# Kernel tuning notes

Hardware: AMD Instinct MI355X
Metric: run time of the kernel (lower is better)

Reference implementation:

```python
import math
import jax, jax.numpy as jnp
import numpy as np

B, T, E, H = 8, 2048, 512, 8
NQ_H, NL = 4, 2          # qubits per attention head, circuit layers
NQ_F, FFN = 8, 2048      # FFN qubits, ffn_dim

# ---- batched state-vector quantum simulation -------------------------------
# state shape: [N, 2, 2, ..., 2] (one axis of size 2 per qubit; wire q = axis q+1)

def apply_ry(state, q, theta):
    """RY(theta) on wire q. theta: scalar or [N] (per-batch angle)."""
    th = jnp.asarray(theta) * 0.5
    c, s = jnp.cos(th), jnp.sin(th)
    if th.ndim == 1:
        shp = (-1,) + (1,) * (state.ndim - 2)
        c, s = c.reshape(shp), s.reshape(shp)
    s0 = jax.lax.index_in_dim(state, 0, axis=q + 1, keepdims=False)
    s1 = jax.lax.index_in_dim(state, 1, axis=q + 1, keepdims=False)
    return jnp.stack([c * s0 - s * s1, s * s0 + c * s1], axis=q + 1)

def apply_cnot(state, ctrl, tgt):
    c0 = jax.lax.index_in_dim(state, 0, axis=ctrl + 1, keepdims=True)
    c1 = jax.lax.index_in_dim(state, 1, axis=ctrl + 1, keepdims=True)
    c1 = jnp.flip(c1, axis=tgt + 1)  # X on target when control = 1
    return jnp.concatenate([c0, c1], axis=ctrl + 1)

def run_circuit(x, params):
    """x: [N, n] data angles. params: [L, n] (shared) or [N, L, n] (per-element).
    Circuit: L x (RY(params) layer + CNOT chain + ring CNOT), then RY(x), then <Z_q>.
    Returns [N, n] PauliZ expectations."""
    N, n = x.shape
    L = params.shape[-2]
    state = jnp.zeros((N, 2 ** n), x.dtype).at[:, 0].set(1.0).reshape((N,) + (2,) * n)
    for l in range(L):
        for q in range(n):
            theta = params[:, l, q] if params.ndim == 3 else params[l, q]
            state = apply_ry(state, q, theta)
        for q in range(n - 1):
            state = apply_cnot(state, q, q + 1)
        state = apply_cnot(state, n - 1, 0)
    for q in range(n):
        state = apply_ry(state, q, x[:, q])
    probs = (state ** 2).reshape(N, 2 ** n)
    bits = (jnp.arange(2 ** n)[:, None] >> (n - 1 - jnp.arange(n))) & 1  # wire 0 = MSB
    return probs @ (1 - 2 * bits).astype(x.dtype)  # [N, n]

def layer_norm(x, g, b, eps=1e-5):
    m = x.mean(-1, keepdims=True)
    v = ((x - m) ** 2).mean(-1, keepdims=True)
    return (x - m) / jnp.sqrt(v + eps) * g + b

def setup_inputs() -> dict:
    key = jax.random.key(0)
    ks = jax.random.split(key, 9)
    def lin(k, o, i):
        return jax.random.normal(k, (o, i), jnp.float32) / np.sqrt(i).astype(np.float32)
    return {
        "x": jax.random.normal(ks[0], (B, T, E), jnp.float32),
        "wq": lin(ks[1], E, E), "wk": lin(ks[2], E, E),
        "wv": lin(ks[3], E, E), "wo": lin(ks[4], E, E),
        "head_params": jax.random.normal(ks[5], (H, NL, NQ_H), jnp.float32),
        "ffn_params": jax.random.normal(ks[6], (2, NQ_F), jnp.float32),
        "w1": lin(ks[7], FFN, NQ_F), "w2": lin(ks[8], E, FFN),
        "g1": jnp.ones((E,), jnp.float32), "b1": jnp.zeros((E,), jnp.float32),
        "g2": jnp.ones((E,), jnp.float32), "b2": jnp.zeros((E,), jnp.float32),
    }

def reference(x, wq, wk, wv, wo, head_params, ffn_params, w1, w2, g1, b1, g2, b2):
    Bb, Tt, Ee = x.shape
    hd = Ee // H
    BT = Bb * Tt
    # ---- quantum multi-head attention (dropout = eval/identity) ----
    q = x @ wq.T; k = x @ wk.T; v = x @ wv.T
    scores = jnp.einsum('bte,bse->bts', q, k) / math.sqrt(Ee)  # NOTE: scale by sqrt(E)
    attn = jax.nn.softmax(scores, axis=-1)
    out = jnp.einsum('bts,bse->bte', attn, v)                  # [B,T,E]
    oh = out.reshape(Bb, Tt, H, hd)
    # fold heads into the batch dim; per-head params broadcast per element
    xh = oh[..., :NQ_H].transpose(2, 0, 1, 3).reshape(H * BT, NQ_H)
    ph = jnp.broadcast_to(head_params[:, None], (H, BT, NL, NQ_H)).reshape(H * BT, NL, NQ_H)
    qout = run_circuit(xh, ph)                                  # [H*BT, NQ_H]
    qout = jnp.pad(qout, ((0, 0), (0, hd - NQ_H)))              # zero-pad to head_dim
    qout = qout.reshape(H, Bb, Tt, hd).transpose(1, 2, 0, 3).reshape(Bb, Tt, Ee)
    attn_out = qout @ wo.T
    x1 = layer_norm(x + attn_out, g1, b1)
    # ---- quantum FFN (only ffn_params[0] used, as in source) ----
    xf = x1.reshape(BT, Ee)[:, :NQ_F]
    f = run_circuit(xf, ffn_params[:1]).reshape(Bb, Tt, NQ_F)
    f = jax.nn.relu(f @ w1.T) @ w2.T
    return layer_norm(x1 + f, g2, b2)
```

## Files before the change

kernel.cpp:

```cpp
#include <hip/hip_runtime.h>
#include <hip/hip_bf16.h>
#include <math.h>


#define B_   8
#define T_   2048
#define E_   512

typedef __attribute__((ext_vector_type(8))) short bf16x8;
typedef __attribute__((ext_vector_type(4))) short bf16x4;
typedef __attribute__((ext_vector_type(4))) float f32x4;

#define GLL16(g, l) __builtin_amdgcn_global_load_lds((const __attribute__((address_space(1))) void*)(g), (__attribute__((address_space(3))) void*)(l), 16, 0, 0)

__device__ inline unsigned short f2bf(float f){
  union { float f; unsigned u; } v; v.f = f;
  unsigned r = v.u + 0x7fff + ((v.u >> 16) & 1);
  return (unsigned short)(r >> 16);
}

__global__ __launch_bounds__(256) void k0_setup(const float* __restrict__ hp,
                         const float* __restrict__ fp,
                         const float* __restrict__ wo, float* __restrict__ cAB,
                         unsigned short* __restrict__ wo32b) {
  int t = threadIdx.x, bi = blockIdx.x;
  if (bi > 0) {
    int gid = (bi-1)*256 + t;
    int e = gid >> 3, c4 = gid & 7;
    float4 v = *(const float4*)(wo + (size_t)e*512 + c4*64);
    unsigned short h[4] = { f2bf(v.x), f2bf(v.y), f2bf(v.z), f2bf(v.w) };
    *(unsigned long long*)(wo32b + (size_t)e*32 + c4*4) = *(unsigned long long*)h;
    return;
  }
  __shared__ float fst[256], tmp[256], ra[256], rb[256];
  fst[t] = (t == 0) ? 1.f : 0.f;
  __syncthreads();
  #pragma unroll
  for (int q = 0; q < 8; ++q) {
    int str = 1 << (7-q);
    float th = 0.5f * fp[q];
    float c = cosf(th), s = sinf(th);
    float self = fst[t], part = fst[t ^ str];
    float nv = (t & str) ? (c*self + s*part) : (c*self - s*part);
    __syncthreads();
    tmp[t] = nv;
    __syncthreads();
    fst[t] = tmp[t];
    __syncthreads();
  }
  #pragma unroll
  for (int g = 0; g < 8; ++g) {
    int ctrl = (g < 7) ? g : 7, tgt = (g < 7) ? g+1 : 0;
    int cs = 1 << (7-ctrl), tsr = 1 << (7-tgt);
    float nv = fst[(t & cs) ? (t ^ tsr) : t];
    __syncthreads();
    fst[t] = nv;
    __syncthreads();
  }
  #pragma unroll
  for (int q = 0; q < 8; ++q) {
    int str = 1 << (7-q);
    float a = fst[t]*fst[t] * ((t & str) ? -1.f : 1.f);
    float b = fst[t]*fst[t ^ str];
    ra[t] = a; rb[t] = b;
    __syncthreads();
    for (int off = 128; off > 0; off >>= 1){
      if (t < off){ ra[t] += ra[t+off]; rb[t] += rb[t+off]; }
      __syncthreads();
    }
    if (t == 0){ cAB[64+q] = ra[0]; cAB[72+q] = rb[0]; }
    __syncthreads();
  }
  if (t < 8) {
    float st[16];
    #pragma unroll
    for (int i=0;i<16;i++) st[i]=0.f;
    st[0]=1.f;
    for (int l=0;l<2;l++){
      for (int q=0;q<4;q++){
        float th = 0.5f*hp[t*8 + l*4 + q];
        float c = cosf(th), s = sinf(th);
        int str = 1<<(3-q);
        for (int i=0;i<16;i++) if (!(i & str)) {
          float s0=st[i], s1=st[i|str];
          st[i]     = c*s0 - s*s1;
          st[i|str] = s*s0 + c*s1;
        }
      }
      for (int q=0;q<4;q++){
        int ctrl = (q<3)? q : 3, tgt = (q<3)? q+1 : 0;
        int cs = 1<<(3-ctrl), tsr = 1<<(3-tgt);
        for (int i=0;i<16;i++) if ((i&cs) && !(i&tsr)) {
          float tt = st[i]; st[i]=st[i|tsr]; st[i|tsr]=tt;
        }
      }
    }
    for (int q=0;q<4;q++){
      int str = 1<<(3-q);
      float A=0.f, Bv=0.f;
      for (int i=0;i<16;i++){
        A  += st[i]*st[i] * ((i&str)? -1.f : 1.f);
        Bv += st[i]*st[i^str];
      }
      cAB[t*4+q]    = A;
      cAB[32+t*4+q] = Bv;
    }
  }
}

__global__ __launch_bounds__(256) void kc_cast(const float* __restrict__ x,
                     const float* __restrict__ wq, const float* __restrict__ wk,
                     const float* __restrict__ w2, unsigned short* __restrict__ xb,
                     unsigned short* __restrict__ wqkb, unsigned short* __restrict__ w2b){
  int bi = blockIdx.x;
  if (bi < 4096) {
    int i = bi*256 + threadIdx.x;
    const float4* p = (const float4*)x + (size_t)i*2;
    float4 a = p[0], b = p[1];
    union { unsigned short h[8]; uint4 u; } o;
    o.h[0]=f2bf(a.x); o.h[1]=f2bf(a.y); o.h[2]=f2bf(a.z); o.h[3]=f2bf(a.w);
    o.h[4]=f2bf(b.x); o.h[5]=f2bf(b.y); o.h[6]=f2bf(b.z); o.h[7]=f2bf(b.w);
    ((uint4*)xb)[i] = o.u;
    return;
  }
  int i = (bi-4096)*256 + threadIdx.x;
  const float* src; unsigned short* dst; float s = 1.f;
  if (i < 65536){
    int row = i >> 6, c8 = (i & 63)*8;
    if (row < 512){ src = wq + (size_t)row*512 + c8; s = 0.044194173824159216f; }
    else          { src = wk + (size_t)(row-512)*512 + c8; }
    dst = wqkb + (size_t)row*512 + c8;
  } else {
    int j = i - 65536;
    src = w2 + (size_t)j*8; dst = w2b + (size_t)j*8;
  }
  float4 a = *(const float4*)src, b = *(const float4*)(src+4);
  union { unsigned short h[8]; uint4 u; } o;
  o.h[0]=f2bf(a.x*s); o.h[1]=f2bf(a.y*s); o.h[2]=f2bf(a.z*s); o.h[3]=f2bf(a.w*s);
  o.h[4]=f2bf(b.x*s); o.h[5]=f2bf(b.y*s); o.h[6]=f2bf(b.z*s); o.h[7]=f2bf(b.w*s);
  *(uint4*)dst = o.u;
}

template<int K, int LDC, bool OUTBF, int GX, int GM>
__global__ __launch_bounds__(256,2) void gemm_bt(
    const unsigned short* __restrict__ A, const unsigned short* __restrict__ Bw,
    void* __restrict__ C, int m_base){
  __shared__ __align__(16) char sm[16384];
  char* As = sm; char* Bs = sm + 8192;
  int t = threadIdx.x, w = t>>6, l = t&63;
  int lr = l&15, quad = l>>4;
  int lin = blockIdx.x;
  int n0 = ((lin >> 3) % GX) * 128;
  int m0 = ((lin & 7) * (GM/8) + lin / (8*GX)) * 128;
  int wr = (w>>1)*64, wc = (w&1)*64;
  f32x4 acc[4][4] = {};
  for (int k0 = 0; k0 < K; k0 += 32){
    __syncthreads();
    #pragma unroll
    for (int c = 0; c < 2; ++c){
      int ch = c*256 + t, row = ch>>2, sw = ch&3, lc = sw ^ ((row>>1)&3);
      GLL16(A  + (size_t)(m0+row)*K + k0 + lc*8, As + c*4096 + w*1024);
      GLL16(Bw + (size_t)(n0+row)*K + k0 + lc*8, Bs + c*4096 + w*1024);
    }
    __syncthreads();
    bf16x8 af[4], bg[4];
    #pragma unroll
    for (int i=0;i<4;++i){
      int ra = wr + i*16 + lr;
      af[i] = *(const bf16x8*)(As + ra*64 + (quad ^ ((ra>>1)&3))*16);
      int rb = wc + i*16 + lr;
      bg[i] = *(const bf16x8*)(Bs + rb*64 + (quad ^ ((rb>>1)&3))*16);
    }
    #pragma unroll
    for (int i=0;i<4;++i)
      #pragma unroll
      for (int j=0;j<4;++j)
        acc[i][j] = __builtin_amdgcn_mfma_f32_16x16x32_bf16(af[i], bg[j], acc[i][j], 0,0,0);
  }
  #pragma unroll
  for (int i=0;i<4;++i)
    #pragma unroll
    for (int j=0;j<4;++j)
      #pragma unroll
      for (int r=0;r<4;++r){
        size_t row = (size_t)(m_base + m0 + wr + i*16 + quad*4 + r);
        int col = n0 + wc + j*16 + lr;
        if constexpr (OUTBF) ((unsigned short*)C)[row*LDC + col] = f2bf(acc[i][j][r]);
        else                 ((float*)C)[row*LDC + col] = acc[i][j][r];
      }
}

__global__ __launch_bounds__(256) void k1_v32(const float* __restrict__ x,
    const float* __restrict__ wv, unsigned short* __restrict__ v32t) {
  int m0 = blockIdx.x * 64;
  __shared__ float Xs[64][36];
  __shared__ float Ws[32][36];
  int t = threadIdx.x;
  int m = t >> 2, c0 = (t & 3) * 8;
  float acc[8] = {};
  for (int k0 = 0; k0 < 512; k0 += 32) {
    #pragma unroll
    for (int u=0; u<2; u++){
      int idx = t + u*256;
      int r = idx >> 3, c4 = (idx & 7) * 4;
      *(float4*)&Xs[r][c4] = *(const float4*)(x + (size_t)(m0+r)*512 + k0 + c4);
    }
    { int r = t >> 3, c4 = (t & 7) * 4;
      int wrow = (r>>2)*64 + (r&3);
      *(float4*)&Ws[r][c4] = *(const float4*)(wv + (size_t)wrow*512 + k0 + c4);
    }
    __syncthreads();
    #pragma unroll
    for (int kk=0; kk<32; kk++){
      float xv = Xs[m][kk];
      #pragma unroll
      for (int j=0;j<8;j++) acc[j] += xv * Ws[c0+j][kk];
    }
    __syncthreads();
  }
  int tok = m0 + m, bb = tok >> 11, s = tok & 2047;
  #pragma unroll
  for (int j=0;j<8;j++)
    v32t[((size_t)(bb*32 + c0 + j))*2048 + s] = f2bf(acc[j]);
}

__global__ __launch_bounds__(256,1) void k2_attn(
    const unsigned short* __restrict__ qkb, const unsigned short* __restrict__ v32t,
    float* __restrict__ Opart, float* __restrict__ mlb){
  __shared__ __align__(16) char sm[57856];
  char* Qc  = sm;
  char* Ks  = sm + 8192;
  char* Vts = sm + 40960;
  float* OtL = (float*)sm;
  float* mL  = (float*)(sm + 36864);
  float* lL  = (float*)(sm + 37888);

  int t = threadIdx.x, w = t>>6, l = t&63;
  int lr = l & 15, quad = l >> 4;
  int lin = blockIdx.x;
  int b = lin & 7;
  int m0 = ((lin >> 3) & 31) * 64;
  int half = lin >> 8;
  size_t bT = (size_t)b*2048;
  const char* qbase = (const char*)qkb + (bT + m0)*2048;
  const char* vbase = (const char*)v32t + (size_t)b*32*4096;

  f32x4 Ot[2][4] = {};
  float mold[4] = {-1e30f,-1e30f,-1e30f,-1e30f};
  float lsum[4] = {0.f,0.f,0.f,0.f};

  for (int step = half*4; step < half*4 + 4; ++step){
    int s0 = step*256;
    const char* kbase = (const char*)qkb + (bT + s0)*2048 + 1024;
    __syncthreads();
    {
      int j = t>>3, seg = t&7;
      const uint4* vs = (const uint4*)(vbase + (size_t)j*4096 + (s0 + seg*32)*2);
      uint4* vd = (uint4*)(Vts + j*528 + seg*64);
      vd[0]=vs[0]; vd[1]=vs[1]; vd[2]=vs[2]; vd[3]=vs[3];
    }
    f32x4 acc[4][4] = {};
    for (int ec = 0; ec < 8; ++ec){
      __syncthreads();
      { int row = t>>2, sw = t&3, lc = sw ^ ((row>>1)&3);
        GLL16(qbase + (size_t)row*2048 + ec*128 +      lc*16, Qc +        w*1024);
        GLL16(qbase + (size_t)row*2048 + ec*128 + 64 + lc*16, Qc + 4096 + w*1024);
      }
      #pragma unroll
      for (int rd = 0; rd < 4; ++rd){
        int ch = rd*256 + t, row = ch>>2, sw = ch&3, lc = sw ^ ((row>>1)&3);
        GLL16(kbase + (size_t)row*2048 + ec*128 +      lc*16, Ks +         rd*4096 + w*1024);
        GLL16(kbase + (size_t)row*2048 + ec*128 + 64 + lc*16, Ks + 16384 + rd*4096 + w*1024);
      }
      __syncthreads();
      #pragma unroll
      for (int kk = 0; kk < 2; ++kk){
        bf16x8 af[4], bq[4];
        #pragma unroll
        for (int si = 0; si < 4; ++si){
          int row = w*64 + si*16 + lr;
          af[si] = *(const bf16x8*)(Ks + kk*16384 + row*64 + (quad ^ ((row>>1)&3))*16);
        }
        #pragma unroll
        for (int qj = 0; qj < 4; ++qj){
          int row = qj*16 + lr;
          bq[qj] = *(const bf16x8*)(Qc + kk*4096 + row*64 + (quad ^ ((row>>1)&3))*16);
        }
        #pragma unroll
        for (int si = 0; si < 4; ++si)
          #pragma unroll
          for (int qj = 0; qj < 4; ++qj)
            acc[si][qj] = __builtin_amdgcn_mfma_f32_16x16x32_bf16(af[si], bq[qj], acc[si][qj], 0,0,0);
      }
    }
    bf16x4 aV[2][4];
    #pragma unroll
    for (int vt=0; vt<2; ++vt)
      #pragma unroll
      for (int si=0; si<4; ++si)
        aV[vt][si] = *(const bf16x4*)(Vts + (vt*16+lr)*528 + (w*64 + si*16 + quad*4)*2);
    #pragma unroll
    for (int qj=0; qj<4; ++qj){
      float mt = -1e30f;
      #pragma unroll
      for (int si=0; si<4; ++si)
        #pragma unroll
        for (int r=0;r<4;++r) mt = fmaxf(mt, acc[si][qj][r]);
      mt = fmaxf(mt, __shfl_xor(mt, 16));
      mt = fmaxf(mt, __shfl_xor(mt, 32));
      float mn = fmaxf(mold[qj], mt);
      float al = __expf(mold[qj] - mn);
      mold[qj] = mn;
      float rs = 0.f;
      #pragma unroll
      for (int si=0; si<4; ++si)
        #pragma unroll
        for (int r=0;r<4;++r){
          float p = __expf(acc[si][qj][r] - mn);
          acc[si][qj][r] = p; rs += p;
        }
      rs += __shfl_xor(rs, 16); rs += __shfl_xor(rs, 32);
      lsum[qj] = lsum[qj]*al + rs;
      Ot[0][qj] *= al; Ot[1][qj] *= al;
      #pragma unroll
      for (int si=0; si<4; ++si){
        bf16x4 pb;
        pb[0]=(short)f2bf(acc[si][qj][0]); pb[1]=(short)f2bf(acc[si][qj][1]);
        pb[2]=(short)f2bf(acc[si][qj][2]); pb[3]=(short)f2bf(acc[si][qj][3]);
        Ot[0][qj] = __builtin_amdgcn_mfma_f32_16x16x16bf16_1k(aV[0][si], pb, Ot[0][qj], 0,0,0);
        Ot[1][qj] = __builtin_amdgcn_mfma_f32_16x16x16bf16_1k(aV[1][si], pb, Ot[1][qj], 0,0,0);
      }
    }
  }
  __syncthreads();
  #pragma unroll
  for (int qj=0; qj<4; ++qj){
    if (quad == 0){ mL[w*64 + qj*16 + lr] = mold[qj]; lL[w*64 + qj*16 + lr] = lsum[qj]; }
    *(f32x4*)(OtL + (size_t)(w*64 + qj*16 + lr)*36 + quad*4)      = Ot[0][qj];
    *(f32x4*)(OtL + (size_t)(w*64 + qj*16 + lr)*36 + 16 + quad*4) = Ot[1][qj];
  }
  __syncthreads();
  {
    int qr = t>>2, vg = (t&3)*8;
    float M = -1e30f;
    #pragma unroll
    for (int w4=0; w4<4; ++w4) M = fmaxf(M, mL[w4*64+qr]);
    float L = 0.f; float o[8] = {};
    #pragma unroll
    for (int w4=0; w4<4; ++w4){
      float a = __expf(mL[w4*64+qr] - M);
      L += a * lL[w4*64+qr];
      const float* Op = OtL + (size_t)(w4*64+qr)*36 + vg;
      #pragma unroll
      for (int j=0;j<8;++j) o[j] += a*Op[j];
    }
    size_t tok = bT + m0 + qr;
    float* od = Opart + ((size_t)half*16384 + tok)*32 + vg;
    *(float4*)od     = make_float4(o[0],o[1],o[2],o[3]);
    *(float4*)(od+4) = make_float4(o[4],o[5],o[6],o[7]);
    if ((t&3) == 0){
      mlb[((size_t)half*16384 + tok)*2]     = M;
      mlb[((size_t)half*16384 + tok)*2 + 1] = L;
    }
  }
}

__global__ __launch_bounds__(256) void k2_merge(const float* __restrict__ Opart,
    const float* __restrict__ mlb, const float* __restrict__ cAB,
    unsigned short* __restrict__ q32b){
  int g = blockIdx.x*256 + threadIdx.x;
  int tok = g >> 2, vg = (g & 3) * 8;
  float m0v = mlb[(size_t)tok*2],           l0 = mlb[(size_t)tok*2 + 1];
  float m1v = mlb[(size_t)(16384+tok)*2],   l1 = mlb[(size_t)(16384+tok)*2 + 1];
  float M = fmaxf(m0v, m1v);
  float a0 = __expf(m0v - M), a1 = __expf(m1v - M);
  float inv = 1.f / (a0*l0 + a1*l1);
  const float* O0 = Opart + (size_t)tok*32 + vg;
  const float* O1 = Opart + (size_t)(16384+tok)*32 + vg;
  union { unsigned short h[8]; uint4 u; } res;
  #pragma unroll
  for (int j=0;j<8;++j){
    float ov = (a0*O0[j] + a1*O1[j]) * inv;
    int cc = vg + j;
    res.h[j] = f2bf(cosf(ov)*cAB[cc] - sinf(ov)*cAB[32+cc]);
  }
  *(uint4*)(q32b + (size_t)tok*32 + vg) = res.u;
}

__global__ __launch_bounds__(256) void k3_proj_ln(const float* __restrict__ x,
    const unsigned short* __restrict__ q32b, const unsigned short* __restrict__ wo32b,
    const float* __restrict__ g1, const float* __restrict__ b1,
    const float* __restrict__ cAB, float* __restrict__ x1, float* __restrict__ fbuf) {
  __shared__ __align__(16) char sm3[36224];
  char* Ws = sm3;
  char* Qs = sm3 + 32768;
  float* red1 = (float*)(sm3 + 34816);
  float* red2 = (float*)(sm3 + 35328);
  float* mm   = (float*)(sm3 + 35840);
  float* rr   = (float*)(sm3 + 35968);
  int t = threadIdx.x, w = t>>6, l = t&63, lr = l&15, quad = l>>4;
  int tok0 = blockIdx.x * 32;
  #pragma unroll
  for (int i=0;i<8;++i){
    int g = t + i*256, row = g>>2, ch = g&3;
    uint4 v = ((const uint4*)wo32b)[g];
    *(uint4*)(Ws + row*64 + (ch ^ ((row>>1)&3))*16) = v;
  }
  if (t < 128){
    int row = t>>2, ch = t&3;
    uint4 v = ((const uint4*)(q32b + (size_t)tok0*32))[t];
    *(uint4*)(Qs + row*64 + (ch ^ ((row>>1)&3))*16) = v;
  }
  __syncthreads();
  bf16x8 af[2], bf[8];
  #pragma unroll
  for (int i=0;i<2;++i){
    int m = i*16 + lr;
    af[i] = *(const bf16x8*)(Qs + m*64 + (quad ^ ((m>>1)&3))*16);
  }
  #pragma unroll
  for (int j=0;j<8;++j){
    int n = w*128 + j*16 + lr;
    bf[j] = *(const bf16x8*)(Ws + n*64 + (quad ^ ((n>>1)&3))*16);
  }
  f32x4 acc[2][8];
  #pragma unroll
  for (int i=0;i<2;++i)
    #pragma unroll
    for (int j=0;j<8;++j){
      f32x4 z = {0.f,0.f,0.f,0.f};
      acc[i][j] = __builtin_amdgcn_mfma_f32_16x16x32_bf16(af[i], bf[j], z, 0,0,0);
    }
  float s1[2][4] = {}, s2[2][4] = {};
  #pragma unroll
  for (int i=0;i<2;++i)
    #pragma unroll
    for (int r=0;r<4;++r){
      int m = i*16 + quad*4 + r;
      const float* xrow = x + (size_t)(tok0+m)*512 + w*128 + lr;
      #pragma unroll
      for (int j=0;j<8;++j){
        float v = acc[i][j][r] + xrow[j*16];
        acc[i][j][r] = v;
        s1[i][r] += v; s2[i][r] += v*v;
      }
    }
  #pragma unroll
  for (int off=1; off<16; off<<=1){
    #pragma unroll
    for (int i=0;i<2;++i)
      #pragma unroll
      for (int r=0;r<4;++r){
        s1[i][r] += __shfl_xor(s1[i][r], off);
        s2[i][r] += __shfl_xor(s2[i][r], off);
      }
  }
  if (lr == 0){
    #pragma unroll
    for (int i=0;i<2;++i)
      #pragma unroll
      for (int r=0;r<4;++r){
        int m = i*16 + quad*4 + r;
        red1[w*32 + m] = s1[i][r];
        red2[w*32 + m] = s2[i][r];
      }
  }
  __syncthreads();
  if (t < 32){
    float a = red1[t] + red1[32+t] + red1[64+t] + red1[96+t];
    float bb = red2[t] + red2[32+t] + red2[64+t] + red2[96+t];
    float mean = a * (1.f/512.f);
    float var  = bb * (1.f/512.f) - mean*mean;
    mm[t] = mean; rr[t] = rsqrtf(var + 1e-5f);
  }
  __syncthreads();
  float g1v[8], b1v[8];
  #pragma unroll
  for (int j=0;j<8;++j){
    int n = w*128 + j*16 + lr;
    g1v[j] = g1[n]; b1v[j] = b1[n];
  }
  #pragma unroll
  for (int i=0;i<2;++i)
    #pragma unroll
    for (int r=0;r<4;++r){
      int m = i*16 + quad*4 + r;
      float mean = mm[m], rstd = rr[m];
      float* orow = x1 + (size_t)(tok0+m)*512 + w*128 + lr;
      #pragma unroll
      for (int j=0;j<8;++j){
        float nv = (acc[i][j][r]-mean)*rstd*g1v[j] + b1v[j];
        orow[j*16] = nv;
        if (w == 0 && j == 0 && lr < 8)
          fbuf[(size_t)(tok0+m)*8 + lr] = cosf(nv)*cAB[64+lr] - sinf(nv)*cAB[72+lr];
      }
    }
}

__global__ __launch_bounds__(512,2) void k4_ffn(
    const float* __restrict__ fbuf, const float* __restrict__ w1,
    const unsigned short* __restrict__ w2b, float* __restrict__ C){
  __shared__ __align__(16) char sm4[40192];
  char* As = sm4;
  char* Bs = sm4 + 4096;
  float* w1s = (float*)(sm4 + 36864);
  int t = threadIdx.x, w = t>>6, l = t&63;
  int lr = l&15, quad = l>>4;
  int m0 = blockIdx.x * 64;
  int am = t>>3, cg = t&7;
  const float4* fp4 = (const float4*)(fbuf + (size_t)(m0 + am)*8);
  float4 fa = fp4[0], fb = fp4[1];
  if (t < 64){
    int row = t>>1, hf = t&1;
    float4 v = *(const float4*)(w1 + row*8 + hf*4);
    *(float4*)(w1s + row*12 + (row>>2)*4 + hf*4) = v;
  }
  f32x4 acc[4][4] = {};
  __syncthreads();
  for (int s = 0; s < 64; ++s){
    int k0 = s*32;
    const float* wcur = w1s + (s&1)*416;
    float*       wnxt = w1s + ((s+1)&1)*416;
    #pragma unroll
    for (int c = 0; c < 4; ++c){
      int ch = c*512 + t, row = ch>>2, sw = ch&3, lc = sw ^ ((row>>1)&3);
      GLL16(w2b + (size_t)row*2048 + k0 + lc*8, Bs + c*8192 + w*1024);
    }
    float4 vn = {0.f,0.f,0.f,0.f};
    if (t < 64 && s < 63){
      int row = t>>1, hf = t&1;
      vn = *(const float4*)(w1 + (size_t)(k0 + 32 + row)*8 + hf*4);
    }
    {
      bf16x4 hb;
      const float* wp = wcur + cg*52;
      #pragma unroll
      for (int j=0;j<4;++j){
        float4 wa = *(const float4*)(wp + j*12);
        float4 wb = *(const float4*)(wp + j*12 + 4);
        float sa = fa.x*wa.x + fa.y*wa.y + fa.z*wa.z + fa.w*wa.w
                 + fb.x*wb.x + fb.y*wb.y + fb.z*wb.z + fb.w*wb.w;
        hb[j] = (short)f2bf(fmaxf(sa, 0.f));
      }
      *(bf16x4*)(As + am*64 + (((cg>>1) ^ ((am>>1)&3))<<4) + ((cg&1)<<3)) = hb;
    }
    if (t < 64 && s < 63){
      int row = t>>1, hf = t&1;
      *(float4*)(wnxt + row*12 + (row>>2)*4 + hf*4) = vn;
    }
    __syncthreads();
    bf16x8 af[4], bg[4];
    #pragma unroll
    for (int i=0;i<4;++i){
      int ra = i*16 + lr;
      af[i] = *(const bf16x8*)(As + ra*64 + (quad ^ ((ra>>1)&3))*16);
      int rb = w*64 + i*16 + lr;
      bg[i] = *(const bf16x8*)(Bs + rb*64 + (quad ^ ((rb>>1)&3))*16);
    }
    #pragma unroll
    for (int i=0;i<4;++i)
      #pragma unroll
      for (int j=0;j<4;++j)
        acc[i][j] = __builtin_amdgcn_mfma_f32_16x16x32_bf16(af[i], bg[j], acc[i][j], 0,0,0);
    __syncthreads();
  }
  #pragma unroll
  for (int i=0;i<4;++i)
    #pragma unroll
    for (int j=0;j<4;++j)
      #pragma unroll
      for (int r=0;r<4;++r){
        size_t row = (size_t)(m0 + i*16 + quad*4 + r);
        int col = w*64 + j*16 + lr;
        C[row*512 + col] = acc[i][j][r];
      }
}

__global__ __launch_bounds__(256) void k5_ln2(const float* __restrict__ x1,
    const float* __restrict__ g2, const float* __restrict__ b2,
    float* __restrict__ out) {
  int tok = blockIdx.x, t = threadIdx.x;
  __shared__ float rs1[4], rs2[4], mv[2];
  float vals[2], ssum=0.f, ssq=0.f;
  #pragma unroll
  for (int u=0;u<2;u++){
    int e = t + u*256;
    float s = x1[(size_t)tok*512 + e] + out[(size_t)tok*512 + e];
    vals[u]=s; ssum+=s; ssq+=s*s;
  }
  #pragma unroll
  for (int off=32; off>0; off>>=1){ ssum += __shfl_down(ssum,off); ssq += __shfl_down(ssq,off); }
  int wid = t >> 6;
  if ((t & 63) == 0){ rs1[wid]=ssum; rs2[wid]=ssq; }
  __syncthreads();
  if (t == 0){
    float a = rs1[0]+rs1[1]+rs1[2]+rs1[3];
    float b = rs2[0]+rs2[1]+rs2[2]+rs2[3];
    float mean = a * (1.f/512.f);
    float var  = b * (1.f/512.f) - mean*mean;
    mv[0]=mean; mv[1]=rsqrtf(var + 1e-5f);
  }
  __syncthreads();
  float mean=mv[0], rstd=mv[1];
  #pragma unroll
  for (int u=0;u<2;u++){
    int e = t + u*256;
    out[(size_t)tok*512 + e] = (vals[u]-mean)*rstd*g2[e] + b2[e];
  }
}

extern "C" void kernel_launch(void* const* d_in, const int* in_sizes, int n_in,
                              void* d_out, int out_size, void* d_ws, size_t ws_size,
                              hipStream_t stream) {
  const float* x  = (const float*)d_in[0];
  const float* wq = (const float*)d_in[1];
  const float* wk = (const float*)d_in[2];
  const float* wv = (const float*)d_in[3];
  const float* wo = (const float*)d_in[4];
  const float* hp = (const float*)d_in[5];
  const float* fp = (const float*)d_in[6];
  const float* w1 = (const float*)d_in[7];
  const float* w2 = (const float*)d_in[8];
  const float* g1 = (const float*)d_in[9];
  const float* b1 = (const float*)d_in[10];
  const float* g2 = (const float*)d_in[11];
  const float* b2 = (const float*)d_in[12];
  float* out = (float*)d_out;
  float* ws  = (float*)d_ws;

  unsigned short* qkb  = (unsigned short*)(ws);
  float*          x1   = ws + 8388608;
  unsigned short* xb   = (unsigned short*)(ws + 16777216);
  unsigned short* wqkb = (unsigned short*)(ws + 20971520);
  unsigned short* w2b  = (unsigned short*)(ws + 21233664);
  unsigned short* v32t = (unsigned short*)(ws + 21757952);
  unsigned short* q32b = (unsigned short*)(ws + 22020096);
  float*          fbuf = ws + 22544384;
  unsigned short* wo32b= (unsigned short*)(ws + 22675456);
  float*          cAB  = ws + 22691840;
  float*          Opart= ws + 22691968;
  float*          mlb  = ws + 23740544;

  k0_setup<<<17, 256, 0, stream>>>(hp, fp, wo, cAB, wo32b);
  kc_cast<<<4864, 256, 0, stream>>>(x, wq, wk, w2, xb, wqkb, w2b);
  gemm_bt<512,1024,true,8,128><<<1024, 256, 0, stream>>>(xb, wqkb, qkb, 0);
  k1_v32<<<256, 256, 0, stream>>>(x, wv, v32t);
  k2_attn<<<512, 256, 0, stream>>>(qkb, v32t, Opart, mlb);
  k2_merge<<<256, 256, 0, stream>>>(Opart, mlb, cAB, q32b);
  k3_proj_ln<<<512, 256, 0, stream>>>(x, q32b, wo32b, g1, b1, cAB, x1, fbuf);
  k4_ffn<<<256, 512, 0, stream>>>(fbuf, w1, w2b, out);
  k5_ln2<<<16384, 256, 0, stream>>>(x1, g2, b2, out);
}
```

Before: 408.5 us.

## Double-buffer FFN GEMM tiles and preload all of w1 into LDS

k4_ffn now double-buffers both the W2 tile (async global-to-LDS loads) and the relu(f·W1) A tile. Step s+1 is prefetched and computed while the MFMAs consume step s, which drops one barrier per iteration. The whole w1 matrix is staged into LDS once up front with padded rows, replacing the per-iteration w1 fetch. LDS use grows to about 152 KB per block, so only one block fits per CU instead of several. That loss of occupancy may offset the overlap gain.

Result: slower. 419.2 us (+2.6%).

```diff
diff --git a/kernel.cpp b/kernel.cpp
--- a/kernel.cpp
+++ b/kernel.cpp
@@ -500,62 +500,71 @@
 __global__ __launch_bounds__(512,2) void k4_ffn(
     const float* __restrict__ fbuf, const float* __restrict__ w1,
     const unsigned short* __restrict__ w2b, float* __restrict__ C){
-  __shared__ __align__(16) char sm4[40192];
-  char* As = sm4;
-  char* Bs = sm4 + 4096;
-  float* w1s = (float*)(sm4 + 36864);
+  __shared__ __align__(16) char sm4[155648];
+  char* Bs  = sm4;
+  char* As  = sm4 + 65536;
+  float* w1f = (float*)(sm4 + 73728);
   int t = threadIdx.x, w = t>>6, l = t&63;
   int lr = l&15, quad = l>>4;
   int m0 = blockIdx.x * 64;
   int am = t>>3, cg = t&7;
+  #pragma unroll
+  for (int c = 0; c < 4; ++c){
+    int ch = c*512 + t, row = ch>>2, sw = ch&3, lc = sw ^ ((row>>1)&3);
+    GLL16(w2b + (size_t)row*2048 + lc*8, Bs + c*8192 + w*1024);
+  }
+  #pragma unroll
+  for (int u=0; u<4; ++u){
+    int r = t*4 + u;
+    float4 a = *(const float4*)(w1 + (size_t)r*8);
+    float4 b = *(const float4*)(w1 + (size_t)r*8 + 4);
+    *(float4*)(w1f + r*10)     = a;
+    *(float4*)(w1f + r*10 + 4) = b;
+  }
   const float4* fp4 = (const float4*)(fbuf + (size_t)(m0 + am)*8);
   float4 fa = fp4[0], fb = fp4[1];
-  if (t < 64){
-    int row = t>>1, hf = t&1;
-    float4 v = *(const float4*)(w1 + row*8 + hf*4);
-    *(float4*)(w1s + row*12 + (row>>2)*4 + hf*4) = v;
-  }
+  __syncthreads();
+  {
+    bf16x4 hb;
+    #pragma unroll
+    for (int j=0;j<4;++j){
+      const float* wp = w1f + (size_t)(cg*4 + j)*10;
+      float4 wa = *(const float4*)wp, wb = *(const float4*)(wp+4);
+      float sa = fa.x*wa.x + fa.y*wa.y + fa.z*wa.z + fa.w*wa.w
+               + fb.x*wb.x + fb.y*wb.y + fb.z*wb.z + fb.w*wb.w;
+      hb[j] = (short)f2bf(fmaxf(sa, 0.f));
+    }
+    *(bf16x4*)(As + am*64 + (((cg>>1) ^ ((am>>1)&3))<<4) + ((cg&1)<<3)) = hb;
+  }
+  __syncthreads();
   f32x4 acc[4][4] = {};
-  __syncthreads();
   for (int s = 0; s < 64; ++s){
-    int k0 = s*32;
-    const float* wcur = w1s + (s&1)*416;
-    float*       wnxt = w1s + ((s+1)&1)*416;
-    #pragma unroll
-    for (int c = 0; c < 4; ++c){
-      int ch = c*512 + t, row = ch>>2, sw = ch&3, lc = sw ^ ((row>>1)&3);
-      GLL16(w2b + (size_t)row*2048 + k0 + lc*8, Bs + c*8192 + w*1024);
-    }
-    float4 vn = {0.f,0.f,0.f,0.f};
-    if (t < 64 && s < 63){
-      int row = t>>1, hf = t&1;
-      vn = *(const float4*)(w1 + (size_t)(k0 + 32 + row)*8 + hf*4);
-    }
-    {
+    int cur = s&1, nxt = cur^1;
+    if (s < 63){
+      int k0 = (s+1)*32;
+      #pragma unroll
+      for (int c = 0; c < 4; ++c){
+        int ch = c*512 + t, row = ch>>2, sw = ch&3, lc = sw ^ ((row>>1)&3);
+        GLL16(w2b + (size_t)row*2048 + k0 + lc*8, Bs + nxt*32768 + c*8192 + w*1024);
+      }
       bf16x4 hb;
-      const float* wp = wcur + cg*52;
       #pragma unroll
       for (int j=0;j<4;++j){
-        float4 wa = *(const float4*)(wp + j*12);
-        float4 wb = *(const float4*)(wp + j*12 + 4);
+        const float* wp = w1f + (size_t)(k0 + cg*4 + j)*10;
+        float4 wa = *(const float4*)wp, wb = *(const float4*)(wp+4);
         float sa = fa.x*wa.x + fa.y*wa.y + fa.z*wa.z + fa.w*wa.w
                  + fb.x*wb.x + fb.y*wb.y + fb.z*wb.z + fb.w*wb.w;
         hb[j] = (short)f2bf(fmaxf(sa, 0.f));
       }
-      *(bf16x4*)(As + am*64 + (((cg>>1) ^ ((am>>1)&3))<<4) + ((cg&1)<<3)) = hb;
-    }
-    if (t < 64 && s < 63){
-      int row = t>>1, hf = t&1;
-      *(float4*)(wnxt + row*12 + (row>>2)*4 + hf*4) = vn;
-    }
-    __syncthreads();
+      *(bf16x4*)(As + nxt*4096 + am*64 + (((cg>>1) ^ ((am>>1)&3))<<4) + ((cg&1)<<3)) = hb;
+    }
     bf16x8 af[4], bg[4];
     #pragma unroll
     for (int i=0;i<4;++i){
       int ra = i*16 + lr;
-      af[i] = *(const bf16x8*)(As + ra*64 + (quad ^ ((ra>>1)&3))*16);
+      af[i] = *(const bf16x8*)(As + cur*4096 + ra*64 + (quad ^ ((ra>>1)&3))*16);
       int rb = w*64 + i*16 + lr;
-      bg[i] = *(const bf16x8*)(Bs + rb*64 + (quad ^ ((rb>>1)&3))*16);
+      bg[i] = *(const bf16x8*)(Bs + cur*32768 + rb*64 + (quad ^ ((rb>>1)&3))*16);
     }
     #pragma unroll
     for (int i=0;i<4;++i)
```
